# Performance work log

Hardware: AMD Instinct MI355X
Metric: run time of the kernel (lower is better)

## Reference

```python
import jax, jax.numpy as jnp
import numpy as np

NODE = 112
B = 4096
L1, L2, L3, L4 = 256, 256, 128, 64


def setup_inputs() -> dict:
    key = jax.random.key(0)
    ks = jax.random.split(key, 13)
    def lin(kw, kb, fan_in, fan_out):
        bound = 1.0 / np.sqrt(fan_in)
        W = jax.random.uniform(kw, (fan_out, fan_in), jnp.float32, -bound, bound)
        b = jax.random.uniform(kb, (fan_out,), jnp.float32, -bound, bound)
        return W, b
    x = jax.random.normal(ks[0], (B, NODE, NODE), jnp.float32)
    W1, b1 = lin(ks[1], ks[2], NODE, L1)
    W2, b2 = lin(ks[3], ks[4], L1, L2)
    W3, b3 = lin(ks[5], ks[6], L2, L3)
    W4, b4 = lin(ks[7], ks[8], L3, L4)
    W5, b5 = lin(ks[9], ks[10], L4, 1)
    Wf, bf = lin(ks[11], ks[12], NODE, 1)
    return {"x": x, "W1": W1, "b1": b1, "W2": W2, "b2": b2,
            "W3": W3, "b3": b3, "W4": W4, "b4": b4,
            "W5": W5, "b5": b5, "Wf": Wf, "bf": bf}


def reference(x, W1, b1, W2, b2, W3, b3, W4, b4, W5, b5, Wf, bf):
    # bmm(x, eye) == x, so first aggregation is the identity on x.
    h = x  # [B, node, node]
    # layer: aggregate via x, project, relu
    def layer(h, W, b):
        h = jnp.einsum('bnm,bmd->bnd', x, h)  # adjacency aggregation
        return jax.nn.relu(h @ W.T + b)
    h = jax.nn.relu(h @ W1.T + b1)            # first bmm is identity
    h = layer(h, W2, b2)
    h = layer(h, W3, b3)
    h = layer(h, W4, b4)
    h = layer(h, W5, b5)                      # [B, node, 1]
    h = h.reshape(h.shape[0], -1)             # [B, node]
    return h @ Wf.T + bf                      # [B, 1]
```

## Files before the change

kernel.cpp:

```cpp
#include <hip/hip_runtime.h>
#include <hip/hip_bf16.h>


#define NODE 112
#define NBATCH 4096
#define SXS 136
#define SAB 264
#define AB1_OFF 29568
#define SMEM_BYTES (2*112*SAB*2)

typedef float  f4v   __attribute__((ext_vector_type(4)));
typedef float  f16v  __attribute__((ext_vector_type(16)));
typedef __bf16 bf8v  __attribute__((ext_vector_type(8)));
typedef short  s8v   __attribute__((ext_vector_type(8)));
typedef unsigned u4v __attribute__((ext_vector_type(4)));
typedef unsigned short ushort_t;

__device__ __forceinline__ ushort_t f2bf(float f) {
  union { float f; unsigned u; } v; v.f = f;
  unsigned r = v.u + 0x7FFFu + ((v.u >> 16) & 1u);
  return (ushort_t)(r >> 16);
}
__device__ __forceinline__ float bf2f(ushort_t h) {
  union { unsigned u; float f; } v; v.u = ((unsigned)h) << 16; return v.f;
}
__device__ __forceinline__ unsigned pk2(float a, float b) {
  unsigned short ul = __builtin_bit_cast(unsigned short, (__bf16)a);
  unsigned short uh = __builtin_bit_cast(unsigned short, (__bf16)b);
  return (unsigned)ul | ((unsigned)uh << 16);
}
__device__ __forceinline__ bf8v ld_frag(const ushort_t* p) {
  s8v t = *(const s8v*)p;
  return __builtin_bit_cast(bf8v, t);
}
__device__ __forceinline__ unsigned xchg32(unsigned v, int lane) {
  return (unsigned)__builtin_amdgcn_ds_bpermute(((lane ^ 32) << 2), (int)v);
}
#define MFMA32(a,b,c) __builtin_amdgcn_mfma_f32_32x32x16_bf16((a),(b),(c),0,0,0)

__device__ __forceinline__ void exch_build(const f16v* acc, float bv, int lane,
                                           unsigned* fr)
{
  const bool hiH = (lane >> 5) != 0;
  #pragma unroll
  for (int m=0;m<4;m++) {
    unsigned P[4][2];
    const int NQ = (m==3) ? 2 : 4;
    #pragma unroll
    for (int q=0;q<4;q++) {
      if (q >= NQ) break;
      float v0 = fmaxf(acc[m][4*q+0]+bv, 0.f);
      float v1 = fmaxf(acc[m][4*q+1]+bv, 0.f);
      float v2 = fmaxf(acc[m][4*q+2]+bv, 0.f);
      float v3 = fmaxf(acc[m][4*q+3]+bv, 0.f);
      P[q][0] = pk2(v0, v1);
      P[q][1] = pk2(v2, v3);
    }
    {
      unsigned s0 = hiH ? P[0][0] : P[1][0];
      unsigned s1 = hiH ? P[0][1] : P[1][1];
      unsigned r0 = xchg32(s0, lane);
      unsigned r1 = xchg32(s1, lane);
      unsigned o0 = hiH ? P[1][0] : P[0][0];
      unsigned o1 = hiH ? P[1][1] : P[0][1];
      fr[8*m+0] = hiH ? r0 : o0;
      fr[8*m+1] = hiH ? r1 : o1;
      fr[8*m+2] = hiH ? o0 : r0;
      fr[8*m+3] = hiH ? o1 : r1;
    }
    if (m < 3) {
      unsigned s0 = hiH ? P[2][0] : P[3][0];
      unsigned s1 = hiH ? P[2][1] : P[3][1];
      unsigned r0 = xchg32(s0, lane);
      unsigned r1 = xchg32(s1, lane);
      unsigned o0 = hiH ? P[3][0] : P[2][0];
      unsigned o1 = hiH ? P[3][1] : P[2][1];
      fr[8*m+4] = hiH ? r0 : o0;
      fr[8*m+5] = hiH ? r1 : o1;
      fr[8*m+6] = hiH ? o0 : r0;
      fr[8*m+7] = hiH ? o1 : r1;
    }
  }
}

__device__ __forceinline__ void proj1_exch(
    const bf8v* Xr, const ushort_t* __restrict__ Wg,
    const float* __restrict__ bias, int nt, int lane, unsigned* fr)
{
  const int l31 = lane & 31, h32 = lane >> 5;
  f16v acc[4];
  #pragma unroll
  for (int m=0;m<4;m++)
    #pragma unroll
    for (int r=0;r<16;r++) acc[m][r] = 0.f;

  const ushort_t* bP = Wg + (nt*32 + l31)*112 + h32*8;
  #pragma unroll
  for (int ks=0; ks<7; ks++) {
    bf8v B = ld_frag(bP + ks*16);
    #pragma unroll
    for (int m=0;m<4;m++)
      acc[m] = MFMA32(Xr[m*7+ks], B, acc[m]);
  }
  exch_build(acc, bias[nt*32 + l31], lane, fr);
}

template<int KS>
__device__ __forceinline__ void proj_exch(
    const ushort_t* aSrc, const ushort_t* __restrict__ Wg, int WK,
    const float* __restrict__ bias, int nt, int lane, unsigned* fr)
{
  const int l31 = lane & 31, h32 = lane >> 5;
  f16v acc[4];
  #pragma unroll
  for (int m=0;m<4;m++)
    #pragma unroll
    for (int r=0;r<16;r++) acc[m][r] = 0.f;

  const ushort_t* aP  = aSrc + l31*SAB + h32*8;
  const ushort_t* aP3 = aSrc + (96 + (l31 & 15))*SAB + h32*8;
  const ushort_t* bP  = Wg + (nt*32 + l31)*WK + h32*8;
  #pragma unroll
  for (int ks=0; ks<KS; ks++) {
    bf8v B = ld_frag(bP + ks*16);
    acc[0] = MFMA32(ld_frag(aP +            ks*16), B, acc[0]);
    acc[1] = MFMA32(ld_frag(aP + 32*SAB +   ks*16), B, acc[1]);
    acc[2] = MFMA32(ld_frag(aP + 64*SAB +   ks*16), B, acc[2]);
    acc[3] = MFMA32(ld_frag(aP3 +           ks*16), B, acc[3]);
  }
  exch_build(acc, bias[nt*32 + l31], lane, fr);
}

__device__ __forceinline__ void agg_store(
    const unsigned* fr, const bf8v* Xr, ushort_t* aDst, int mt, int lane)
{
  const int l31 = lane & 31, h32 = lane >> 5;
  f16v acc[4];
  #pragma unroll
  for (int n=0;n<4;n++)
    #pragma unroll
    for (int r=0;r<16;r++) acc[n][r] = 0.f;

  #pragma unroll
  for (int ks=0; ks<7; ks++) {
    u4v t = (u4v){fr[4*ks+0], fr[4*ks+1], fr[4*ks+2], fr[4*ks+3]};
    bf8v A = __builtin_bit_cast(bf8v, t);
    #pragma unroll
    for (int n=0;n<4;n++)
      acc[n] = MFMA32(A, Xr[n*7+ks], acc[n]);
  }

  #pragma unroll
  for (int n=0;n<4;n++) {
    ushort_t* arow = aDst + (n*32 + l31)*SAB;
    bool on = (n < 3) || (l31 < 16);
    #pragma unroll
    for (int q=0;q<4;q++) {
      uint2 pv;
      pv.x = pk2(acc[n][4*q+0], acc[n][4*q+1]);
      pv.y = pk2(acc[n][4*q+2], acc[n][4*q+3]);
      if (on) *(uint2*)(arow + mt*32 + 8*q + 4*h32) = pv;
    }
  }
}

__global__ void prep_weights(const float* __restrict__ W1, const float* __restrict__ W2,
                             const float* __restrict__ W3, const float* __restrict__ W4,
                             ushort_t* __restrict__ o)
{
  int i = blockIdx.x*256 + threadIdx.x;
  if (i < 28672)       o[i] = f2bf(W1[i]);
  else if (i < 94208)  o[i] = f2bf(W2[i - 28672]);
  else if (i < 126976) o[i] = f2bf(W3[i - 94208]);
  else if (i < 135168) o[i] = f2bf(W4[i - 126976]);
}

__global__ void __launch_bounds__(512, 2) gcn_kernel(
    const float* __restrict__ x, const ushort_t* __restrict__ wsp,
    const float* __restrict__ b1, const float* __restrict__ b2,
    const float* __restrict__ b3, const float* __restrict__ b4,
    const float* __restrict__ W5, const float* __restrict__ b5,
    const float* __restrict__ Wf, const float* __restrict__ bfc,
    float* __restrict__ out)
{
  extern __shared__ ushort_t smem[];
  ushort_t* aB0 = smem;
  ushort_t* aB1 = smem + AB1_OFF;

  const int tid  = threadIdx.x;
  const int w    = tid >> 6;
  const int lane = tid & 63;
  const int l31  = lane & 31, h32 = lane >> 5;

  {
    ushort_t* Xstg = aB1;
    const float4* x4 = (const float4*)(x + (size_t)blockIdx.x * (NODE*NODE));
    for (int i = tid; i < (NODE*NODE/4); i += 512) {
      float4 v = x4[i];
      int r = i / 28, c4 = (i - r*28) * 4;
      uint2 pv; pv.x = pk2(v.x, v.y); pv.y = pk2(v.z, v.w);
      *(uint2*)(Xstg + r*SXS + c4) = pv;
    }
  }
  __syncthreads();

  bf8v Xr[28];
  {
    const ushort_t* Xstg = aB1;
    #pragma unroll
    for (int t=0;t<4;t++) {
      int row = (t < 3) ? (t*32 + l31) : (96 + (l31 & 15));
      const ushort_t* rp = Xstg + row*SXS + h32*8;
      #pragma unroll
      for (int ks=0;ks<7;ks++)
        Xr[t*7+ks] = ld_frag(rp + ks*16);
    }
  }
  __syncthreads();

  unsigned fr[28];

  proj1_exch(Xr, wsp, b1, w, lane, fr);
  agg_store(fr, Xr, aB0, w, lane);
  __syncthreads();

  proj_exch<16>(aB0, wsp + 28672, 256, b2, w, lane, fr);
  agg_store(fr, Xr, aB1, w, lane);
  __syncthreads();

  if (w < 4) {
    proj_exch<16>(aB1, wsp + 94208, 256, b3, w, lane, fr);
    agg_store(fr, Xr, aB0, w, lane);
  }
  __syncthreads();

  if (w < 2) {
    proj_exch<8>(aB0, wsp + 126976, 128, b4, w, lane, fr);
    agg_store(fr, Xr, aB1, w, lane);
  }
  __syncthreads();

  float partial = 0.f;
  if (tid < NODE) {
    const ushort_t* row = aB1 + tid*SAB;
    float s = 0.f;
    #pragma unroll
    for (int k4 = 0; k4 < 16; k4++) {
      uint2 u = *(const uint2*)(row + k4*4);
      s += bf2f((ushort_t)(u.x & 0xFFFF)) * W5[k4*4+0];
      s += bf2f((ushort_t)(u.x >> 16))    * W5[k4*4+1];
      s += bf2f((ushort_t)(u.y & 0xFFFF)) * W5[k4*4+2];
      s += bf2f((ushort_t)(u.y >> 16))    * W5[k4*4+3];
    }
    s += b5[0];
    s = s > 0.f ? s : 0.f;
    partial = s * Wf[tid];
  }
  float* red = (float*)aB0;
  __syncthreads();
  if (tid < 128) red[tid] = partial;
  __syncthreads();
  if (w == 0) {
    float v = red[lane] + red[lane + 64];
    #pragma unroll
    for (int off = 32; off > 0; off >>= 1)
      v += __shfl_xor(v, off, 64);
    if (lane == 0) out[blockIdx.x] = v + bfc[0];
  }
}

extern "C" void kernel_launch(void* const* d_in, const int* in_sizes, int n_in,
                              void* d_out, int out_size, void* d_ws, size_t ws_size,
                              hipStream_t stream) {
  const float* x   = (const float*)d_in[0];
  const float* W1  = (const float*)d_in[1];
  const float* b1  = (const float*)d_in[2];
  const float* W2  = (const float*)d_in[3];
  const float* b2  = (const float*)d_in[4];
  const float* W3  = (const float*)d_in[5];
  const float* b3  = (const float*)d_in[6];
  const float* W4  = (const float*)d_in[7];
  const float* b4  = (const float*)d_in[8];
  const float* W5  = (const float*)d_in[9];
  const float* b5  = (const float*)d_in[10];
  const float* Wf  = (const float*)d_in[11];
  const float* bfc = (const float*)d_in[12];
  ushort_t* wsp = (ushort_t*)d_ws;
  float* out = (float*)d_out;

  prep_weights<<<528, 256, 0, stream>>>(W1, W2, W3, W4, wsp);

  (void)hipFuncSetAttribute((const void*)gcn_kernel,
                            hipFuncAttributeMaxDynamicSharedMemorySize, SMEM_BYTES);
  gcn_kernel<<<NBATCH, 512, SMEM_BYTES, stream>>>(x, wsp, b1, b2, b3, b4,
                                                  W5, b5, Wf, bfc, out);
}
```

Measured before the change: 568.5 us.

## Single swizzled LDS activation buffer and LDS-resident X to raise occupancy

Replaces the two padded ping-pong activation buffers with one unpadded, XOR-swizzled 112x256 buffer. The first 96 rows of X move out of registers into LDS, so only the last row tile stays in registers. Aggregation is split into two-accumulator halves to lower register pressure, and launch bounds go from 2 to 4 blocks per CU. This cuts LDS and VGPR use to fit more blocks per CU, at the cost of extra LDS reads of X and extra barriers between projection and aggregation, since the buffer is now reused in place.

```diff
diff --git a/kernel.cpp b/kernel.cpp
--- a/kernel.cpp
+++ b/kernel.cpp
@@ -4,10 +4,9 @@
 
 #define NODE 112
 #define NBATCH 4096
-#define SXS 136
-#define SAB 264
-#define AB1_OFF 29568
-#define SMEM_BYTES (2*112*SAB*2)
+#define SXS 120
+#define AB_OFF (96*SXS)
+#define SMEM_BYTES ((AB_OFF + 112*256)*2)
 
 typedef float  f4v   __attribute__((ext_vector_type(4)));
 typedef float  f16v  __attribute__((ext_vector_type(16)));
@@ -84,7 +83,7 @@
 }
 
 __device__ __forceinline__ void proj1_exch(
-    const bf8v* Xr, const ushort_t* __restrict__ Wg,
+    const ushort_t* Xs, const bf8v* Xr3, const ushort_t* __restrict__ Wg,
     const float* __restrict__ bias, int nt, int lane, unsigned* fr)
 {
   const int l31 = lane & 31, h32 = lane >> 5;
@@ -94,21 +93,23 @@
     #pragma unroll
     for (int r=0;r<16;r++) acc[m][r] = 0.f;
 
+  const ushort_t* aP = Xs + l31*SXS + h32*8;
   const ushort_t* bP = Wg + (nt*32 + l31)*112 + h32*8;
   #pragma unroll
   for (int ks=0; ks<7; ks++) {
     bf8v B = ld_frag(bP + ks*16);
-    #pragma unroll
-    for (int m=0;m<4;m++)
-      acc[m] = MFMA32(Xr[m*7+ks], B, acc[m]);
+    acc[0] = MFMA32(ld_frag(aP +          ks*16), B, acc[0]);
+    acc[1] = MFMA32(ld_frag(aP + 32*SXS + ks*16), B, acc[1]);
+    acc[2] = MFMA32(ld_frag(aP + 64*SXS + ks*16), B, acc[2]);
+    acc[3] = MFMA32(Xr3[ks], B, acc[3]);
   }
   exch_build(acc, bias[nt*32 + l31], lane, fr);
 }
 
 template<int KS>
 __device__ __forceinline__ void proj_exch(
-    const ushort_t* aSrc, const ushort_t* __restrict__ Wg, int WK,
-    const float* __restrict__ bias, int nt, int lane, unsigned* fr)
+    const ushort_t* aBs, const ushort_t* __restrict__ Wg, int WK,
+    const float* __restrict__ bias, int nt, int lane, int sw, unsigned* fr)
 {
   const int l31 = lane & 31, h32 = lane >> 5;
   f16v acc[4];
@@ -117,49 +118,55 @@
     #pragma unroll
     for (int r=0;r<16;r++) acc[m][r] = 0.f;
 
-  const ushort_t* aP  = aSrc + l31*SAB + h32*8;
-  const ushort_t* aP3 = aSrc + (96 + (l31 & 15))*SAB + h32*8;
-  const ushort_t* bP  = Wg + (nt*32 + l31)*WK + h32*8;
+  const int r0 = l31*256, r1 = (32+l31)*256, r2 = (64+l31)*256;
+  const int r3 = (96 + (l31 & 15))*256;
+  const ushort_t* bP = Wg + (nt*32 + l31)*WK + h32*8;
   #pragma unroll
   for (int ks=0; ks<KS; ks++) {
     bf8v B = ld_frag(bP + ks*16);
-    acc[0] = MFMA32(ld_frag(aP +            ks*16), B, acc[0]);
-    acc[1] = MFMA32(ld_frag(aP + 32*SAB +   ks*16), B, acc[1]);
-    acc[2] = MFMA32(ld_frag(aP + 64*SAB +   ks*16), B, acc[2]);
-    acc[3] = MFMA32(ld_frag(aP3 +           ks*16), B, acc[3]);
+    const int c = (16*ks + 8*h32) ^ sw;
+    acc[0] = MFMA32(ld_frag(aBs + r0 + c), B, acc[0]);
+    acc[1] = MFMA32(ld_frag(aBs + r1 + c), B, acc[1]);
+    acc[2] = MFMA32(ld_frag(aBs + r2 + c), B, acc[2]);
+    acc[3] = MFMA32(ld_frag(aBs + r3 + c), B, acc[3]);
   }
   exch_build(acc, bias[nt*32 + l31], lane, fr);
 }
 
-__device__ __forceinline__ void agg_store(
-    const unsigned* fr, const bf8v* Xr, ushort_t* aDst, int mt, int lane)
+template<int N0>
+__device__ __forceinline__ void agg_half(
+    const unsigned* fr, const ushort_t* Xs, const bf8v* Xr3,
+    ushort_t* aBs, int mt, int lane, int sw)
 {
   const int l31 = lane & 31, h32 = lane >> 5;
-  f16v acc[4];
-  #pragma unroll
-  for (int n=0;n<4;n++)
-    #pragma unroll
-    for (int r=0;r<16;r++) acc[n][r] = 0.f;
-
+  f16v acc0, acc1;
+  #pragma unroll
+  for (int r=0;r<16;r++) { acc0[r] = 0.f; acc1[r] = 0.f; }
+
+  const ushort_t* bP = Xs + l31*SXS + h32*8;
   #pragma unroll
   for (int ks=0; ks<7; ks++) {
     u4v t = (u4v){fr[4*ks+0], fr[4*ks+1], fr[4*ks+2], fr[4*ks+3]};
     bf8v A = __builtin_bit_cast(bf8v, t);
-    #pragma unroll
-    for (int n=0;n<4;n++)
-      acc[n] = MFMA32(A, Xr[n*7+ks], acc[n]);
-  }
-
-  #pragma unroll
-  for (int n=0;n<4;n++) {
-    ushort_t* arow = aDst + (n*32 + l31)*SAB;
-    bool on = (n < 3) || (l31 < 16);
+    bf8v B0 = ld_frag(bP + N0*32*SXS + ks*16);
+    bf8v B1 = (N0 == 0) ? ld_frag(bP + 32*SXS + ks*16) : Xr3[ks];
+    acc0 = MFMA32(A, B0, acc0);
+    acc1 = MFMA32(A, B1, acc1);
+  }
+
+  #pragma unroll
+  for (int s=0;s<2;s++) {
+    const f16v& a = s ? acc1 : acc0;
+    const int n = N0 + s;
+    const int row = (n < 3) ? (n*32 + l31) : (96 + l31);
+    const bool on = (n < 3) || (l31 < 16);
     #pragma unroll
     for (int q=0;q<4;q++) {
       uint2 pv;
-      pv.x = pk2(acc[n][4*q+0], acc[n][4*q+1]);
-      pv.y = pk2(acc[n][4*q+2], acc[n][4*q+3]);
-      if (on) *(uint2*)(arow + mt*32 + 8*q + 4*h32) = pv;
+      pv.x = pk2(a[4*q+0], a[4*q+1]);
+      pv.y = pk2(a[4*q+2], a[4*q+3]);
+      const int col = (mt*32 + 8*q + 4*h32) ^ sw;
+      if (on) *(uint2*)(aBs + row*256 + col) = pv;
     }
   }
 }
@@ -175,7 +182,7 @@
   else if (i < 135168) o[i] = f2bf(W4[i - 126976]);
 }
 
-__global__ void __launch_bounds__(512, 2) gcn_kernel(
+__global__ void __launch_bounds__(512, 4) gcn_kernel(
     const float* __restrict__ x, const ushort_t* __restrict__ wsp,
     const float* __restrict__ b1, const float* __restrict__ b2,
     const float* __restrict__ b3, const float* __restrict__ b4,
@@ -184,69 +191,72 @@
     float* __restrict__ out)
 {
   extern __shared__ ushort_t smem[];
-  ushort_t* aB0 = smem;
-  ushort_t* aB1 = smem + AB1_OFF;
+  ushort_t* Xs = smem;
+  ushort_t* aB = smem + AB_OFF;
 
   const int tid  = threadIdx.x;
   const int w    = tid >> 6;
   const int lane = tid & 63;
   const int l31  = lane & 31, h32 = lane >> 5;
+  const int sw   = (l31 & 7) << 3;
 
   {
-    ushort_t* Xstg = aB1;
     const float4* x4 = (const float4*)(x + (size_t)blockIdx.x * (NODE*NODE));
     for (int i = tid; i < (NODE*NODE/4); i += 512) {
       float4 v = x4[i];
       int r = i / 28, c4 = (i - r*28) * 4;
       uint2 pv; pv.x = pk2(v.x, v.y); pv.y = pk2(v.z, v.w);
-      *(uint2*)(Xstg + r*SXS + c4) = pv;
-    }
-  }
-  __syncthreads();
-
-  bf8v Xr[28];
+      ushort_t* dst = (r < 96) ? (Xs + r*SXS + c4) : (aB + (r-96)*SXS + c4);
+      *(uint2*)dst = pv;
+    }
+  }
+  __syncthreads();
+
+  bf8v Xr3[7];
   {
-    const ushort_t* Xstg = aB1;
-    #pragma unroll
-    for (int t=0;t<4;t++) {
-      int row = (t < 3) ? (t*32 + l31) : (96 + (l31 & 15));
-      const ushort_t* rp = Xstg + row*SXS + h32*8;
-      #pragma unroll
-      for (int ks=0;ks<7;ks++)
-        Xr[t*7+ks] = ld_frag(rp + ks*16);
-    }
+    const ushort_t* sp = aB + (l31 & 15)*SXS + h32*8;
+    #pragma unroll
+    for (int ks=0;ks<7;ks++) Xr3[ks] = ld_frag(sp + ks*16);
   }
   __syncthreads();
 
   unsigned fr[28];
 
-  proj1_exch(Xr, wsp, b1, w, lane, fr);
-  agg_store(fr, Xr, aB0, w, lane);
-  __syncthreads();
-
-  proj_exch<16>(aB0, wsp + 28672, 256, b2, w, lane, fr);
-  agg_store(fr, Xr, aB1, w, lane);
-  __syncthreads();
-
+  proj1_exch(Xs, Xr3, wsp, b1, w, lane, fr);
+  agg_half<0>(fr, Xs, Xr3, aB, w, lane, sw);
+  agg_half<2>(fr, Xs, Xr3, aB, w, lane, sw);
+  __syncthreads();
+
+  proj_exch<16>(aB, wsp + 28672, 256, b2, w, lane, sw, fr);
+  __syncthreads();
+  agg_half<0>(fr, Xs, Xr3, aB, w, lane, sw);
+  agg_half<2>(fr, Xs, Xr3, aB, w, lane, sw);
+  __syncthreads();
+
+  if (w < 4) proj_exch<16>(aB, wsp + 94208, 256, b3, w, lane, sw, fr);
+  __syncthreads();
   if (w < 4) {
-    proj_exch<16>(aB1, wsp + 94208, 256, b3, w, lane, fr);
-    agg_store(fr, Xr, aB0, w, lane);
-  }
-  __syncthreads();
-
+    agg_half<0>(fr, Xs, Xr3, aB, w, lane, sw);
+    agg_half<2>(fr, Xs, Xr3, aB, w, lane, sw);
+  }
+  __syncthreads();
+
+  if (w < 2) proj_exch<8>(aB, wsp + 126976, 128, b4, w, lane, sw, fr);
+  __syncthreads();
   if (w < 2) {
-    proj_exch<8>(aB0, wsp + 126976, 128, b4, w, lane, fr);
-    agg_store(fr, Xr, aB1, w, lane);
+    agg_half<0>(fr, Xs, Xr3, aB, w, lane, sw);
+    agg_half<2>(fr, Xs, Xr3, aB, w, lane, sw);
   }
   __syncthreads();
 
   float partial = 0.f;
   if (tid < NODE) {
-    const ushort_t* row = aB1 + tid*SAB;
+    const int swr = (tid & 7) << 3;
+    const ushort_t* row = aB + tid*256;
     float s = 0.f;
     #pragma unroll
     for (int k4 = 0; k4 < 16; k4++) {
-      uint2 u = *(const uint2*)(row + k4*4);
+      uint2 u = *(const uint2*)(row + ((4*k4) ^ swr));
       s += bf2f((ushort_t)(u.x & 0xFFFF)) * W5[k4*4+0];
       s += bf2f((ushort_t)(u.x >> 16))    * W5[k4*4+1];
       s += bf2f((ushort_t)(u.y & 0xFFFF)) * W5[k4*4+2];
@@ -256,8 +266,7 @@
     s = s > 0.f ? s : 0.f;
     partial = s * Wf[tid];
   }
-  float* red = (float*)aB0;
-  __syncthreads();
+  float* red = (float*)Xs;
   if (tid < 128) red[tid] = partial;
   __syncthreads();
   if (w == 0) {
```

Result: slower. 618.1 us (+8.7%).
